# Kernel optimization log

Hardware: AMD Instinct MI355X
Metric: run time of the kernel (lower is better)

The kernel has to match this reference:

```python
import jax, jax.numpy as jnp
import numpy as np

EMBED_DIM = 1024
NUM_HEADS = 16
HEAD_DIM = EMBED_DIM // NUM_HEADS


def setup_inputs() -> dict:
    key = jax.random.key(0)
    k_x, k_wqkv, k_bqkv, k_wo, k_bo = jax.random.split(key, 5)
    B, T, C = 4, 2048, EMBED_DIM
    # PyTorch Linear default init scale ~ 1/sqrt(fan_in); use small normals
    s = 1.0 / np.sqrt(C)
    return {
        "x": jax.random.normal(k_x, (B, T, C), dtype=jnp.float32),
        "w_qkv": jax.random.normal(k_wqkv, (C, 3 * C), dtype=jnp.float32) * s,
        "b_qkv": jax.random.normal(k_bqkv, (3 * C,), dtype=jnp.float32) * s,
        "w_out": jax.random.normal(k_wo, (C, C), dtype=jnp.float32) * s,
        "b_out": jax.random.normal(k_bo, (C,), dtype=jnp.float32) * s,
    }


def reference(x, w_qkv, b_qkv, w_out, b_out):
    B, T, C = x.shape
    H, D = NUM_HEADS, HEAD_DIM
    qkv = x @ w_qkv + b_qkv                      # (B, T, 3C)
    q, k, v = jnp.split(qkv, 3, axis=-1)
    # (B, H, T, D)
    q = q.reshape(B, T, H, D).transpose(0, 2, 1, 3)
    k = k.reshape(B, T, H, D).transpose(0, 2, 1, 3)
    v = v.reshape(B, T, H, D).transpose(0, 2, 1, 3)
    scores = jnp.einsum("bhqd,bhkd->bhqk", q, k) / jnp.sqrt(jnp.float32(D))
    causal = jnp.tril(jnp.ones((T, T), dtype=bool))  # (T, T)
    scores = jnp.where(causal[None, None, :, :], scores, -jnp.inf)
    attn = jax.nn.softmax(scores, axis=-1)
    out = jnp.einsum("bhqk,bhkd->bhqd", attn, v)  # (B, H, T, D)
    out = out.transpose(0, 2, 1, 3).reshape(B, T, C)
    return out @ w_out + b_out
```

## Files before the change

kernel.cpp:

```cpp
#include <hip/hip_runtime.h>
#include <hip/hip_bf16.h>

#define B_  4
#define T_  2048
#define C_  1024
#define H_  16
#define D_  64
#define BH_ (B_*H_)

typedef float  f32x4  __attribute__((ext_vector_type(4)));
typedef __bf16 bf16x8 __attribute__((ext_vector_type(8)));
typedef __bf16 bf16x2 __attribute__((ext_vector_type(2)));

static __device__ __forceinline__ ushort f2bf(float f) {
    union { float f; unsigned u; } x; x.f = f;
    unsigned r = ((x.u >> 16) & 1u) + 0x7fffu;
    return (ushort)((x.u + r) >> 16);
}

static __device__ __forceinline__ uint packbf(float a, float b) {
    bf16x2 v = { (__bf16)a, (__bf16)b };
    return __builtin_bit_cast(uint, v);
}

static __device__ __forceinline__ void gload_lds16(const void* g, void* l) {
    __builtin_amdgcn_global_load_lds(
        (const __attribute__((address_space(1))) unsigned int*)g,
        (__attribute__((address_space(3))) unsigned int*)l, 16, 0, 0);
}

template<int N> static __device__ __forceinline__ void waitcnt_vm() {
    if constexpr (N == 0) asm volatile("s_waitcnt vmcnt(0)" ::: "memory");
    else if constexpr (N == 3) asm volatile("s_waitcnt vmcnt(3)" ::: "memory");
    else if constexpr (N == 4) asm volatile("s_waitcnt vmcnt(4)" ::: "memory");
    else static_assert(N == 0 || N == 3 || N == 4);
    __builtin_amdgcn_sched_barrier(0);
}
static __device__ __forceinline__ void lgkm0() {
    asm volatile("s_waitcnt lgkmcnt(0)" ::: "memory");
    __builtin_amdgcn_sched_barrier(0);
}

__global__ void cvt_kernel(const float* __restrict__ in, ushort* __restrict__ out, int n) {
    int i = (blockIdx.x * blockDim.x + threadIdx.x) * 4;
    if (i < n) {
        float4 v = *(const float4*)(in + i);
        ushort4 o;
        o.x = f2bf(v.x); o.y = f2bf(v.y); o.z = f2bf(v.z); o.w = f2bf(v.w);
        *(ushort4*)(out + i) = o;
    }
}

__global__ void transpose_cvt_kernel(const float* __restrict__ in, ushort* __restrict__ out,
                                     int K, int N) {
    __shared__ float tile[32][33];
    int k0 = blockIdx.y * 32, n0 = blockIdx.x * 32;
    int tx = threadIdx.x & 31, ty = threadIdx.x >> 5;
    #pragma unroll
    for (int r = 0; r < 32; r += 8)
        tile[ty + r][tx] = in[(size_t)(k0 + ty + r) * N + n0 + tx];
    __syncthreads();
    #pragma unroll
    for (int r = 0; r < 32; r += 8)
        out[(size_t)(n0 + ty + r) * K + k0 + tx] = f2bf(tile[tx][ty + r]);
}

__global__ void transpose_v_kernel(const ushort* __restrict__ v, ushort* __restrict__ vt) {
    __shared__ ushort tile[64][66];
    int bh = blockIdx.x >> 5;
    int t0 = (blockIdx.x & 31) * 64;
    const ushort* src = v  + ((size_t)bh * T_ + t0) * D_;
    ushort*       dst = vt + (size_t)bh * D_ * T_ + t0;
    int tx = threadIdx.x & 63, ty = threadIdx.x >> 6;
    #pragma unroll
    for (int r = 0; r < 64; r += 4)
        tile[ty + r][tx] = src[(size_t)(ty + r) * D_ + tx];
    __syncthreads();
    #pragma unroll
    for (int r = 0; r < 64; r += 4)
        dst[(size_t)(ty + r) * T_ + tx] = tile[tx][ty + r];
}

template<int NFR, bool QKV>
__global__ __launch_bounds__(512, 2) void gemm_hk(
    const ushort* __restrict__ A,
    const ushort* __restrict__ Bt,
    const float*  __restrict__ bias,
    void* __restrict__ outp)
{
    constexpr int NT   = 16;
    constexpr int BN   = NFR * 64;
    constexpr int ABUF = 32768;
    constexpr int BBUF = BN * 128;
    constexpr int LB   = (NFR == 4) ? 2 : 1;
    constexpr int PK   = 2 + LB;
    __shared__ __align__(16) char lds[2 * ABUF + 2 * BBUF];
    char* ldsB = lds + 2 * ABUF;

    const int m0 = blockIdx.y * 256, n0 = blockIdx.x * BN;
    const int tid = threadIdx.x, lane = tid & 63;
    const int wv = tid >> 6, wm = wv >> 2, wn = wv & 3;
    const int lr = lane & 15, lh = lane >> 4;

    const int sc = (tid & 3) ^ ((tid >> 2) & 3);
    const ushort* aA = A  + (size_t)(m0 + (tid >> 2)) * 1024 + sc * 8;
    const ushort* aB = Bt + (size_t)(n0 + (tid >> 2)) * 1024 + sc * 8;

    const int cxor = (lh ^ (lr & 3)) * 16;
    const int arow = (wm * 128 + lr) * 64 + cxor;
    const int brow = (wn * (NFR * 16) + lr) * 64 + cxor;

    f32x4 acc[8][NFR] = {};

    auto stage_a = [&](int buf, int t, int kh) {
        #pragma unroll
        for (int p = 0; p < 2; ++p)
            gload_lds16(aA + (size_t)p * 131072 + t * 64 + kh * 32,
                        lds + buf * ABUF + kh * 16384 + p * 8192 + tid * 16);
    };
    auto stage_b = [&](int buf, int t, int kh) {
        #pragma unroll
        for (int p = 0; p < LB; ++p)
            gload_lds16(aB + (size_t)p * 131072 + t * 64 + kh * 32,
                        ldsB + buf * BBUF + kh * (BBUF / 2) + p * 8192 + tid * 16);
    };
    auto read_a = [&](bf16x8 (&af)[8], int buf, int kh) {
        const char* base = lds + buf * ABUF + kh * 16384 + arow;
        #pragma unroll
        for (int mi = 0; mi < 8; ++mi) af[mi] = *(const bf16x8*)(base + mi * 1024);
    };
    auto read_b = [&](bf16x8& b0, bf16x8& b1, int buf, int kh, int nh) {
        const char* base = ldsB + buf * BBUF + kh * (BBUF / 2) + brow + nh * 2048;
        b0 = *(const bf16x8*)(base);
        b1 = *(const bf16x8*)(base + 1024);
    };

#define MFMA2(NI, BB0, BB1)                                                          \
    do {                                                                             \
        __builtin_amdgcn_s_setprio(1);                                               \
        _Pragma("unroll")                                                            \
        for (int mi = 0; mi < 8; ++mi) {                                             \
            acc[mi][NI]     = __builtin_amdgcn_mfma_f32_16x16x32_bf16(af[mi], BB0,   \
                                                     acc[mi][NI], 0, 0, 0);          \
            acc[mi][NI + 1] = __builtin_amdgcn_mfma_f32_16x16x32_bf16(af[mi], BB1,   \
                                                     acc[mi][NI + 1], 0, 0, 0);      \
        }                                                                            \
        __builtin_amdgcn_s_setprio(0);                                               \
    } while (0)

    stage_a(0, 0, 0); stage_b(0, 0, 0);
    stage_a(0, 0, 1); stage_b(0, 0, 1);
    waitcnt_vm<PK>();
    __builtin_amdgcn_s_barrier();

    for (int t = 0; t < NT; ++t) {
        const int cur = t & 1, nxt = cur ^ 1;
        const bool pf = (t + 1 < NT);
        bf16x8 af[8], b0, b1;
        if constexpr (NFR == 4) {
            read_a(af, cur, 0); read_b(b0, b1, cur, 0, 0);
            if (pf) stage_a(nxt, t + 1, 0);
            __builtin_amdgcn_s_barrier();
            lgkm0();
            MFMA2(0, b0, b1);
            read_b(b0, b1, cur, 0, 1);
            if (pf) stage_b(nxt, t + 1, 0);
            if (t < NT - 1) waitcnt_vm<4>(); else waitcnt_vm<0>();
            __builtin_amdgcn_s_barrier();
            lgkm0();
            MFMA2(2, b0, b1);
            read_a(af, cur, 1); read_b(b0, b1, cur, 1, 0);
            if (pf) stage_a(nxt, t + 1, 1);
            __builtin_amdgcn_s_barrier();
            lgkm0();
            MFMA2(0, b0, b1);
            read_b(b0, b1, cur, 1, 1);
            if (pf) stage_b(nxt, t + 1, 1);
            if (t < NT - 1) waitcnt_vm<4>();
            __builtin_amdgcn_s_barrier();
            lgkm0();
            MFMA2(2, b0, b1);
        } else {
            read_a(af, cur, 0); read_b(b0, b1, cur, 0, 0);
            if (pf) { stage_a(nxt, t + 1, 0); stage_b(nxt, t + 1, 0); }
            if (t < NT - 1) waitcnt_vm<3>(); else waitcnt_vm<0>();
            __builtin_amdgcn_s_barrier();
            lgkm0();
            MFMA2(0, b0, b1);
            read_a(af, cur, 1); read_b(b0, b1, cur, 1, 0);
            if (pf) { stage_a(nxt, t + 1, 1); stage_b(nxt, t + 1, 1); }
            if (t < NT - 1) waitcnt_vm<3>();
            __builtin_amdgcn_s_barrier();
            lgkm0();
            MFMA2(0, b0, b1);
        }
    }
#undef MFMA2

    #pragma unroll
    for (int mi = 0; mi < 8; ++mi) {
        #pragma unroll
        for (int ni = 0; ni < NFR; ++ni) {
            int col = n0 + wn * (NFR * 16) + ni * 16 + lr;
            float bv = bias[col];
            if constexpr (QKV) {
                ushort* qkv = (ushort*)outp;
                int which = col >> 10;
                int h = (col & 1023) >> 6;
                int d = col & 63;
                #pragma unroll
                for (int r = 0; r < 4; ++r) {
                    int row = m0 + wm * 128 + mi * 16 + lh * 4 + r;
                    int b = row >> 11, tt = row & 2047;
                    float v = acc[mi][ni][r] + bv;
                    if (which == 0) v *= 0.18033688011112042f;
                    qkv[(size_t)which * (BH_ * T_ * D_) +
                        (((size_t)(b * H_ + h)) * T_ + tt) * D_ + d] = f2bf(v);
                }
            } else {
                float* Cout = (float*)outp;
                #pragma unroll
                for (int r = 0; r < 4; ++r) {
                    int row = m0 + wm * 128 + mi * 16 + lh * 4 + r;
                    Cout[(size_t)row * C_ + col] = acc[mi][ni][r] + bv;
                }
            }
        }
    }
}

__global__ __launch_bounds__(256, 4) void flash_kernel(
    const ushort* __restrict__ qb,
    const ushort* __restrict__ kb,
    const ushort* __restrict__ vt,
    ushort* __restrict__ ob)
{
    __shared__ __align__(16) ushort sK[2][64 * 64];
    __shared__ __align__(16) ushort sV[2][64 * 64];
    __shared__ __align__(16) ushort sP[4][16 * 64];
    const int bh  = blockIdx.x >> 4;
    const int pr  = blockIdx.x & 15;
    const int qtA = pr, qtB = 31 - pr;
    const int lane = threadIdx.x & 63, wv = threadIdx.x >> 6;
    const int lr = lane & 15, lh = lane >> 4;

    const ushort* qrowA = qb + ((size_t)bh * T_ + qtA * 64 + wv * 16 + lr) * D_;
    const ushort* qrowB = qb + ((size_t)bh * T_ + qtB * 64 + wv * 16 + lr) * D_;
    bf16x8 qfA0 = *(const bf16x8*)(qrowA + lh * 8);
    bf16x8 qfA1 = *(const bf16x8*)(qrowA + 32 + lh * 8);
    bf16x8 qfB0 = *(const bf16x8*)(qrowB + lh * 8);
    bf16x8 qfB1 = *(const bf16x8*)(qrowB + 32 + lh * 8);

    const int srow = lane >> 3;
    const int scol = ((lane & 7) ^ srow) * 8;
    const ushort* kbase = kb + (size_t)bh * T_ * D_;
    const ushort* vbase = vt + (size_t)bh * D_ * T_;

    const int sw   = (lr & 7) << 4;
    const int off0 = (16 * lh) ^ sw;
    const int off1 = (64 + 16 * lh) ^ sw;

    f32x4 oA[4] = {}, oB[4] = {};
    float mA = -1e30f, lA = 0.f, mB = -1e30f, lB = 0.f;

    auto redmax = [&](float x) {
        x = fmaxf(x, __int_as_float(__builtin_amdgcn_ds_swizzle(__float_as_int(x), 0x401F)));
        x = fmaxf(x, __shfl_xor(x, 32, 64));
        return x;
    };
    auto redsum = [&](float x) {
        x += __int_as_float(__builtin_amdgcn_ds_swizzle(__float_as_int(x), 0x401F));
        x += __shfl_xor(x, 32, 64);
        return x;
    };

    auto tile = [&](f32x4 (&o)[4], float& mrow, float& lsum,
                    const bf16x8& q0f, const bf16x8& q1f,
                    const char* K0, const char* V0, bool diag) {
        f32x4 s[4];
        __builtin_amdgcn_s_setprio(1);
        #pragma unroll
        for (int nt = 0; nt < 4; ++nt) {
            const char* krow = K0 + (nt * 16 + lr) * 128;
            bf16x8 k0 = *(const bf16x8*)(krow + off0);
            bf16x8 k1 = *(const bf16x8*)(krow + off1);
            f32x4 a = {0.f, 0.f, 0.f, 0.f};
            a = __builtin_amdgcn_mfma_f32_16x16x32_bf16(k0, q0f, a, 0, 0, 0);
            a = __builtin_amdgcn_mfma_f32_16x16x32_bf16(k1, q1f, a, 0, 0, 0);
            s[nt] = a;
        }
        __builtin_amdgcn_s_setprio(0);
        if (diag) {
            #pragma unroll
            for (int nt = 0; nt < 4; ++nt)
                #pragma unroll
                for (int r = 0; r < 4; ++r)
                    if (nt * 16 + lh * 4 + r > wv * 16 + lr) s[nt][r] = -INFINITY;
        }

        float pmax = fmaxf(fmaxf(fmaxf(s[0][0], s[0][1]), fmaxf(s[0][2], s[0][3])),
                           fmaxf(fmaxf(s[1][0], s[1][1]), fmaxf(s[1][2], s[1][3])));
        pmax = fmaxf(pmax, fmaxf(fmaxf(fmaxf(s[2][0], s[2][1]), fmaxf(s[2][2], s[2][3])),
                                 fmaxf(fmaxf(s[3][0], s[3][1]), fmaxf(s[3][2], s[3][3]))));
        pmax = redmax(pmax);

        if (__any(pmax > mrow + 8.f)) {
            float mnew = fmaxf(mrow, pmax);
            float al = __builtin_exp2f(mrow - mnew);
            lsum *= al;
            #pragma unroll
            for (int r = 0; r < 4; ++r) {
                float ar = __shfl(al, lh * 20 + r, 64);
                o[0][r] *= ar; o[1][r] *= ar; o[2][r] *= ar; o[3][r] *= ar;
            }
            mrow = mnew;
        }

        float rsum = 0.f;
        uint pk[8];
        #pragma unroll
        for (int nt = 0; nt < 4; ++nt) {
            float p0 = __builtin_exp2f(s[nt][0] - mrow);
            float p1 = __builtin_exp2f(s[nt][1] - mrow);
            float p2 = __builtin_exp2f(s[nt][2] - mrow);
            float p3 = __builtin_exp2f(s[nt][3] - mrow);
            rsum += (p0 + p1) + (p2 + p3);
            pk[nt * 2]     = packbf(p0, p1);
            pk[nt * 2 + 1] = packbf(p2, p3);
        }
        lsum += redsum(rsum);

        char* P = (char*)sP[wv];
        {
            char* prow = P + lr * 128;
            #pragma unroll
            for (int nt = 0; nt < 4; ++nt) {
                uint2 w; w.x = pk[nt * 2]; w.y = pk[nt * 2 + 1];
                *(uint2*)(prow + ((32 * nt + 8 * lh) ^ sw)) = w;
            }
        }
        asm volatile("" ::: "memory");
        bf16x8 pf0 = *(const bf16x8*)(P + lr * 128 + off0);
        bf16x8 pf1 = *(const bf16x8*)(P + lr * 128 + off1);

        __builtin_amdgcn_s_setprio(1);
        #pragma unroll
        for (int dt = 0; dt < 4; ++dt) {
            const char* vrow = V0 + (dt * 16 + lr) * 128;
            bf16x8 v0 = *(const bf16x8*)(vrow + off0);
            bf16x8 v1 = *(const bf16x8*)(vrow + off1);
            o[dt] = __builtin_amdgcn_mfma_f32_16x16x32_bf16(pf0, v0, o[dt], 0, 0, 0);
            o[dt] = __builtin_amdgcn_mfma_f32_16x16x32_bf16(pf1, v1, o[dt], 0, 0, 0);
        }
        __builtin_amdgcn_s_setprio(0);
    };

    #pragma unroll
    for (int i = 0; i < 2; ++i) {
        int j = i * 4 + wv;
        gload_lds16(kbase + (size_t)(j * 8 + srow) * D_ + scol, &sK[0][j * 512]);
        gload_lds16(vbase + (size_t)(j * 8 + srow) * T_ + scol, &sV[0][j * 512]);
    }
    __syncthreads();

    for (int kt = 0; kt <= qtB; ++kt) {
        const int cur = kt & 1;
        if (kt < qtB) {
            const int nb = cur ^ 1;
            #pragma unroll
            for (int i = 0; i < 2; ++i) {
                int j = i * 4 + wv;
                gload_lds16(kbase + (size_t)((kt + 1) * 64 + j * 8 + srow) * D_ + scol, &sK[nb][j * 512]);
                gload_lds16(vbase + (size_t)(j * 8 + srow) * T_ + (kt + 1) * 64 + scol, &sV[nb][j * 512]);
            }
        }
        const char* K0 = (const char*)sK[cur];
        const char* V0 = (const char*)sV[cur];
        if (kt <= qtA) tile(oA, mA, lA, qfA0, qfA1, K0, V0, kt == qtA);
        tile(oB, mB, lB, qfB0, qfB1, K0, V0, kt == qtB);
        __syncthreads();
    }

    const int b = bh >> 4, h = bh & 15;
    auto writeout = [&](f32x4 (&o)[4], float lsum, int q0) {
        float inv = 1.f / lsum;
        #pragma unroll
        for (int r = 0; r < 4; ++r) {
            float ir = __shfl(inv, lh * 20 + r, 64);
            int q = q0 + lh * 4 + r;
            #pragma unroll
            for (int dt = 0; dt < 4; ++dt)
                ob[((size_t)b * T_ + q) * C_ + h * 64 + dt * 16 + lr] = f2bf(o[dt][r] * ir);
        }
    };
    writeout(oA, lA, qtA * 64 + wv * 16);
    writeout(oB, lB, qtB * 64 + wv * 16);
}

extern "C" void kernel_launch(void* const* d_in, const int* in_sizes, int n_in,
                              void* d_out, int out_size, void* d_ws, size_t ws_size,
                              hipStream_t stream) {
    const float* x     = (const float*)d_in[0];
    const float* w_qkv = (const float*)d_in[1];
    const float* b_qkv = (const float*)d_in[2];
    const float* w_out = (const float*)d_in[3];
    const float* b_out = (const float*)d_in[4];
    float* out = (float*)d_out;

    char* ws = (char*)d_ws;
    ushort* xb     = (ushort*)(ws + 0);
    ushort* wqkvT  = (ushort*)(ws + 16777216);
    ushort* woutT  = (ushort*)(ws + 23068672);
    ushort* qkv    = (ushort*)(ws + 25165824);
    ushort* vT     = (ushort*)(ws + 75497472);
    ushort* attn   = xb;
    ushort* qb = qkv;
    ushort* kb = qkv + (size_t)BH_ * T_ * D_;
    ushort* vb = qkv + (size_t)2 * BH_ * T_ * D_;

    const int nx = B_ * T_ * C_;
    cvt_kernel<<<nx / 4 / 256, 256, 0, stream>>>(x, xb, nx);
    transpose_cvt_kernel<<<dim3(3 * C_ / 32, C_ / 32), 256, 0, stream>>>(w_qkv, wqkvT, C_, 3 * C_);
    transpose_cvt_kernel<<<dim3(C_ / 32, C_ / 32), 256, 0, stream>>>(w_out, woutT, C_, C_);
    gemm_hk<2, true><<<dim3(3 * C_ / 128, B_ * T_ / 256), 512, 0, stream>>>(xb, wqkvT, b_qkv, qkv);
    transpose_v_kernel<<<BH_ * (T_ / 64), 256, 0, stream>>>(vb, vT);
    flash_kernel<<<BH_ * 16, 256, 0, stream>>>(qb, kb, vT, attn);
    gemm_hk<2, false><<<dim3(C_ / 128, B_ * T_ / 256), 512, 0, stream>>>(attn, woutT, b_out, out);
}
```

Measured before the change: 208.6 us.

## Fuse V transpose into QKV GEMM epilogue, widen QKV tile, remap blocks for XCDs

```diff
diff --git a/kernel.cpp b/kernel.cpp
--- a/kernel.cpp
+++ b/kernel.cpp
@@ -65,28 +65,13 @@
         out[(size_t)(n0 + ty + r) * K + k0 + tx] = f2bf(tile[tx][ty + r]);
 }
 
-__global__ void transpose_v_kernel(const ushort* __restrict__ v, ushort* __restrict__ vt) {
-    __shared__ ushort tile[64][66];
-    int bh = blockIdx.x >> 5;
-    int t0 = (blockIdx.x & 31) * 64;
-    const ushort* src = v  + ((size_t)bh * T_ + t0) * D_;
-    ushort*       dst = vt + (size_t)bh * D_ * T_ + t0;
-    int tx = threadIdx.x & 63, ty = threadIdx.x >> 6;
-    #pragma unroll
-    for (int r = 0; r < 64; r += 4)
-        tile[ty + r][tx] = src[(size_t)(ty + r) * D_ + tx];
-    __syncthreads();
-    #pragma unroll
-    for (int r = 0; r < 64; r += 4)
-        dst[(size_t)(ty + r) * T_ + tx] = tile[tx][ty + r];
-}
-
 template<int NFR, bool QKV>
 __global__ __launch_bounds__(512, 2) void gemm_hk(
     const ushort* __restrict__ A,
     const ushort* __restrict__ Bt,
     const float*  __restrict__ bias,
-    void* __restrict__ outp)
+    void* __restrict__ outp,
+    ushort* __restrict__ vtp)
 {
     constexpr int NT   = 16;
     constexpr int BN   = NFR * 64;
@@ -97,7 +82,12 @@
     __shared__ __align__(16) char lds[2 * ABUF + 2 * BBUF];
     char* ldsB = lds + 2 * ABUF;
 
-    const int m0 = blockIdx.y * 256, n0 = blockIdx.x * BN;
+    const int gX   = gridDim.x;
+    const int orig = blockIdx.y * gX + blockIdx.x;
+    const int cpx  = (gX * gridDim.y) >> 3;
+    const int wg   = (orig & 7) * cpx + (orig >> 3);
+    const int m0 = (wg / gX) * 256, n0 = (wg % gX) * BN;
+
     const int tid = threadIdx.x, lane = tid & 63;
     const int wv = tid >> 6, wm = wv >> 2, wn = wv & 3;
     const int lr = lane & 15, lh = lane >> 4;
@@ -208,14 +198,24 @@
                 int which = col >> 10;
                 int h = (col & 1023) >> 6;
                 int d = col & 63;
-                #pragma unroll
-                for (int r = 0; r < 4; ++r) {
-                    int row = m0 + wm * 128 + mi * 16 + lh * 4 + r;
-                    int b = row >> 11, tt = row & 2047;
-                    float v = acc[mi][ni][r] + bv;
-                    if (which == 0) v *= 0.18033688011112042f;
-                    qkv[(size_t)which * (BH_ * T_ * D_) +
-                        (((size_t)(b * H_ + h)) * T_ + tt) * D_ + d] = f2bf(v);
+                if (which == 2) {
+                    #pragma unroll
+                    for (int r = 0; r < 4; ++r) {
+                        int row = m0 + wm * 128 + mi * 16 + lh * 4 + r;
+                        int b = row >> 11, tt = row & 2047;
+                        vtp[(((size_t)(b * H_ + h)) * D_ + d) * T_ + tt] =
+                            f2bf(acc[mi][ni][r] + bv);
+                    }
+                } else {
+                    #pragma unroll
+                    for (int r = 0; r < 4; ++r) {
+                        int row = m0 + wm * 128 + mi * 16 + lh * 4 + r;
+                        int b = row >> 11, tt = row & 2047;
+                        float v = acc[mi][ni][r] + bv;
+                        if (which == 0) v *= 0.18033688011112042f;
+                        qkv[(size_t)which * (BH_ * T_ * D_) +
+                            (((size_t)(b * H_ + h)) * T_ + tt) * D_ + d] = f2bf(v);
+                    }
                 }
             } else {
                 float* Cout = (float*)outp;
@@ -238,8 +238,9 @@
     __shared__ __align__(16) ushort sK[2][64 * 64];
     __shared__ __align__(16) ushort sV[2][64 * 64];
     __shared__ __align__(16) ushort sP[4][16 * 64];
-    const int bh  = blockIdx.x >> 4;
-    const int pr  = blockIdx.x & 15;
+    const int wg  = ((blockIdx.x & 7) << 7) | (blockIdx.x >> 3);
+    const int bh  = wg >> 4;
+    const int pr  = wg & 15;
     const int qtA = pr, qtB = 31 - pr;
     const int lane = threadIdx.x & 63, wv = threadIdx.x >> 6;
     const int lr = lane & 15, lh = lane >> 4;
@@ -416,14 +417,12 @@
     ushort* attn   = xb;
     ushort* qb = qkv;
     ushort* kb = qkv + (size_t)BH_ * T_ * D_;
-    ushort* vb = qkv + (size_t)2 * BH_ * T_ * D_;
 
     const int nx = B_ * T_ * C_;
     cvt_kernel<<<nx / 4 / 256, 256, 0, stream>>>(x, xb, nx);
     transpose_cvt_kernel<<<dim3(3 * C_ / 32, C_ / 32), 256, 0, stream>>>(w_qkv, wqkvT, C_, 3 * C_);
     transpose_cvt_kernel<<<dim3(C_ / 32, C_ / 32), 256, 0, stream>>>(w_out, woutT, C_, C_);
-    gemm_hk<2, true><<<dim3(3 * C_ / 128, B_ * T_ / 256), 512, 0, stream>>>(xb, wqkvT, b_qkv, qkv);
-    transpose_v_kernel<<<BH_ * (T_ / 64), 256, 0, stream>>>(vb, vT);
+    gemm_hk<4, true><<<dim3(3 * C_ / 256, B_ * T_ / 256), 512, 0, stream>>>(xb, wqkvT, b_qkv, qkv, vT);
     flash_kernel<<<BH_ * 16, 256, 0, stream>>>(qb, kb, vT, attn);
-    gemm_hk<2, false><<<dim3(C_ / 128, B_ * T_ / 256), 512, 0, stream>>>(attn, woutT, b_out, out);
-}
+    gemm_hk<2, false><<<dim3(C_ / 128, B_ * T_ / 256), 512, 0, stream>>>(attn, woutT, b_out, out, nullptr);
+}
```

Measured after the change: 210.9 us. No clear change (+1.1%).
